# Performance work log

Measured on AMD Instinct MI355X. Metric: run time of the kernel, lower is better.

The kernel has to match this reference:

```python
import jax, jax.numpy as jnp
import numpy as np

N_NODES = 100000
N_EDGES = 1600000
IN_FEATS = 128
HID = 32
N_REL = 5
N_BASES = 2
N_PAIRS = 4096


def setup_inputs() -> dict:
    key = jax.random.key(0)
    ks = jax.random.split(key, 24)
    d = {}
    d['x'] = jax.random.normal(ks[0], (N_NODES, IN_FEATS), dtype=jnp.float32)
    d['edge_mask'] = jnp.ones((N_EDGES,), dtype=jnp.float32)
    d['etype'] = jax.random.randint(ks[1], (N_EDGES,), 0, N_REL, dtype=jnp.int32)
    d['src'] = jax.random.randint(ks[2], (N_EDGES,), 0, N_NODES, dtype=jnp.int32)
    d['dst'] = jax.random.randint(ks[3], (N_EDGES,), 0, N_NODES, dtype=jnp.int32)
    d['users_idx'] = jax.random.randint(ks[4], (N_PAIRS,), 0, N_NODES, dtype=jnp.int32)
    d['items_idx'] = jax.random.randint(ks[5], (N_PAIRS,), 0, N_NODES, dtype=jnp.int32)
    # RelGraphConv params (basis decomposition): layer1 in->32, layers 2,3 32->32
    def s(k, din):
        return 1.0 / np.sqrt(din)
    d['V1'] = jax.random.normal(ks[6], (N_BASES, IN_FEATS, HID), dtype=jnp.float32) * s(0, IN_FEATS)
    d['comp1'] = jax.random.normal(ks[7], (N_REL, N_BASES), dtype=jnp.float32)
    d['loop1'] = jax.random.normal(ks[8], (IN_FEATS, HID), dtype=jnp.float32) * s(0, IN_FEATS)
    d['b1'] = jnp.zeros((HID,), dtype=jnp.float32)
    d['V2'] = jax.random.normal(ks[9], (N_BASES, HID, HID), dtype=jnp.float32) * s(0, HID)
    d['comp2'] = jax.random.normal(ks[10], (N_REL, N_BASES), dtype=jnp.float32)
    d['loop2'] = jax.random.normal(ks[11], (HID, HID), dtype=jnp.float32) * s(0, HID)
    d['b2'] = jnp.zeros((HID,), dtype=jnp.float32)
    d['V3'] = jax.random.normal(ks[12], (N_BASES, HID, HID), dtype=jnp.float32) * s(0, HID)
    d['comp3'] = jax.random.normal(ks[13], (N_REL, N_BASES), dtype=jnp.float32)
    d['loop3'] = jax.random.normal(ks[14], (HID, HID), dtype=jnp.float32) * s(0, HID)
    d['b3'] = jnp.zeros((HID,), dtype=jnp.float32)
    # MLP head: lin1 (2*sum(latent_dim[1:]) = 192 -> 128), lin2 (128 -> 1)
    d['w1'] = jax.random.normal(ks[15], (2 * 3 * HID, 128), dtype=jnp.float32) * (1.0 / np.sqrt(2 * 3 * HID))
    d['bw1'] = jnp.zeros((128,), dtype=jnp.float32)
    d['w2'] = jax.random.normal(ks[16], (128, 1), dtype=jnp.float32) * (1.0 / np.sqrt(128))
    d['bw2'] = jnp.zeros((1,), dtype=jnp.float32)
    return d


def _rgcn_layer(x, V, comp, loopw, bias, etype, src, dst, norm):
    # basis-decomposed relational conv: W_r = sum_b comp[r,b] * V[b]
    xb = jnp.einsum('nd,bdo->nbo', x, V)                       # [N,B,O]
    msg = jnp.einsum('eb,ebo->eo', comp[etype], xb[src])       # [E,O]
    msg = msg * norm[:, None]                                  # edge_mask norm
    agg = jax.ops.segment_sum(msg, dst, num_segments=x.shape[0])
    return jnp.tanh(agg + x @ loopw + bias)


def reference(x, edge_mask, etype, src, dst, users_idx, items_idx,
              V1, comp1, loop1, b1, V2, comp2, loop2, b2, V3, comp3, loop3, b3,
              w1, bw1, w2, bw2):
    h1 = _rgcn_layer(x, V1, comp1, loop1, b1, etype, src, dst, edge_mask)
    h2 = _rgcn_layer(h1, V2, comp2, loop2, b2, etype, src, dst, edge_mask)
    h3 = _rgcn_layer(h2, V3, comp3, loop3, b3, etype, src, dst, edge_mask)
    concat_states = jnp.concatenate([h1, h2, h3], axis=1)      # [N, 96]
    feats = jnp.concatenate([concat_states[users_idx], concat_states[items_idx]], axis=1)  # [P,192]
    hidden = jax.nn.relu(feats @ w1 + bw1)
    out = hidden @ w2 + bw2
    return out[:, 0]  # multiply_by = 1
```

## Files before the change

### kernel.cpp

```cpp
#include <hip/hip_runtime.h>
#include <stdint.h>

#define N_NODES  100000
#define N_EDGES  1600000
#define IN_FEATS 128
#define HID      32
#define N_REL    5
#define N_BASES  2
#define N_PAIRS  4096

#define NB        196
#define BCAP      16384
#define EPB       2048
#define SC_BLOCKS 782
#define WP_BLOCKS 137
#define NBSORT    392
#define TD_BLOCKS 625

typedef __attribute__((ext_vector_type(8))) short short8;
typedef __attribute__((ext_vector_type(4))) float f32x4;

__device__ inline unsigned int pack_bf16(float a, float b) {
    unsigned int ua = __float_as_uint(a), ub = __float_as_uint(b);
    ua = (ua + 0x7fffu + ((ua >> 16) & 1u)) >> 16;
    ub = (ub + 0x7fffu + ((ub >> 16) & 1u)) >> 16;
    return ua | (ub << 16);
}

__device__ inline unsigned short bf16_1(float a) {
    unsigned int u = __float_as_uint(a);
    u = (u + 0x7fffu + ((u >> 16) & 1u)) >> 16;
    return (unsigned short)u;
}

__device__ inline void split_bf16_2(float a, float b, unsigned int& hi, unsigned int& lo) {
    unsigned int ha = bf16_1(a), hb = bf16_1(b);
    hi = ha | (hb << 16);
    float fa = __uint_as_float(ha << 16), fb = __uint_as_float(hb << 16);
    lo = pack_bf16(a - fa, b - fb);
}


#define SMEM_BYTES 23856

__global__ __launch_bounds__(256) void k_scatter_wprep(
    const int* __restrict__ src, const int* __restrict__ dst,
    const int* __restrict__ etype, const float* __restrict__ mask,
    int* __restrict__ gcur, int2* __restrict__ ebuf,
    const float* __restrict__ V1, const float* __restrict__ comp1, const float* __restrict__ loop1,
    const float* __restrict__ V2, const float* __restrict__ loop2,
    const float* __restrict__ V3, const float* __restrict__ loop3,
    unsigned short* __restrict__ Wbf1, unsigned short* __restrict__ Wcat2,
    unsigned short* __restrict__ Wcat3,
    const int* __restrict__ uidx, const int* __restrict__ iidx,
    unsigned char* __restrict__ flags) {
    __shared__ __attribute__((aligned(16))) char smem[SMEM_BYTES];
    int b = blockIdx.x;
    int t = threadIdx.x;
    if (b < SC_BLOCKS) {
        int2*  srec    = (int2*)smem;
        short* sb      = (short*)(smem + 16384);
        int*   lh      = (int*)(smem + 20480);
        int*   lex     = (int*)(smem + 21264);
        int*   gbase   = (int*)(smem + 22048);
        int*   scanbuf = (int*)(smem + 22832);
        int e0 = b * EPB;
        if (t < NB) lh[t] = 0;
        __syncthreads();
        int2 rec[8];
        int  bk[8];
#pragma unroll
        for (int i = 0; i < 8; i++) {
            int e = e0 + t + i * 256;
            if (e < N_EDGES) {
                int d = dst[e];
                bk[i] = d >> 9;
                rec[i].x = ((d & 511) << 23) | (src[e] << 4) | etype[e];
                rec[i].y = __float_as_int(mask[e]);
                atomicAdd(&lh[bk[i]], 1);
            } else bk[i] = -1;
        }
        __syncthreads();
        int cnt = (t < NB) ? lh[t] : 0;
        scanbuf[t] = cnt;
        __syncthreads();
        for (int off = 1; off < 256; off <<= 1) {
            int v = (t >= off) ? scanbuf[t - off] : 0;
            __syncthreads();
            scanbuf[t] += v;
            __syncthreads();
        }
        if (t < NB) {
            lex[t] = scanbuf[t] - cnt;
            gbase[t] = t * BCAP + (cnt ? atomicAdd(&gcur[t], cnt) : 0);
            lh[t] = 0;
        }
        __syncthreads();
#pragma unroll
        for (int i = 0; i < 8; i++) {
            if (bk[i] >= 0) {
                int p = lex[bk[i]] + atomicAdd(&lh[bk[i]], 1);
                srec[p] = rec[i];
                sb[p] = (short)bk[i];
            }
        }
        __syncthreads();
        int total = scanbuf[NB - 1];
        for (int idx = t; idx < total; idx += 256) {
            int bb = sb[idx];
            ebuf[gbase[bb] + (idx - lex[bb])] = srec[idx];
        }
        return;
    }
    int wb = b - SC_BLOCKS;
    if (wb == 136) {
        unsigned int* f4 = (unsigned int*)flags;
        for (int i = t; i < 25000; i += 256) f4[i] = 0u;
        __syncthreads();
        for (int i = t; i < N_PAIRS; i += 256) {
            flags[uidx[i]] = 1;
            flags[iidx[i]] = 1;
        }
        return;
    }
    if (wb < 96) {
        int idx = wb * 256 + t;
        if (idx >= 192 * IN_FEATS) return;
        int j = idx / IN_FEATS, k = idx % IN_FEATS;
        float v;
        if (j < 160) {
            int r = j >> 5, o = j & 31;
            v = comp1[r * 2 + 0] * V1[(size_t)(0 * IN_FEATS + k) * 32 + o]
              + comp1[r * 2 + 1] * V1[(size_t)(1 * IN_FEATS + k) * 32 + o];
        } else {
            v = loop1[k * 32 + (j - 160)];
        }
        Wbf1[idx] = bf16_1(v);
        return;
    }
    const float *V, *loopw;
    unsigned short* Wc;
    int idx;
    if (wb < 116) { V = V2; loopw = loop2; Wc = Wcat2; idx = (wb - 96) * 256 + t; }
    else          { V = V3; loopw = loop3; Wc = Wcat3; idx = (wb - 116) * 256 + t; }
    if (idx >= 32 * 160) return;
    int col = idx / 160, k = idx % 160;
    int seg = k >> 5, inner = k & 31;
    float v;
    if (seg < 2)      v = V[inner * 32 + col];
    else if (seg < 4) v = V[(32 + inner) * 32 + col];
    else              v = loopw[inner * 32 + col];
    Wc[idx] = bf16_1(v);
}


#define SMEM2_BYTES 19456

__global__ __launch_bounds__(512) void k_bsort_tl1(
    const int* __restrict__ gcur, const int2* __restrict__ ebuf,
    int2* __restrict__ esort, int* __restrict__ offsets,
    const float* __restrict__ xin,
    const unsigned short* __restrict__ Wbf, const float* __restrict__ bias,
    unsigned short* __restrict__ xs16, float* __restrict__ aggout) {
    __shared__ __attribute__((aligned(16))) char smem2[SMEM2_BYTES];
    int b = blockIdx.x;
    int t = threadIdx.x;
    if (b < NBSORT) {
        int* hist = (int*)smem2;
        int* incl = (int*)(smem2 + 2048);
        int* cur  = (int*)(smem2 + 4096);
        int* bs   = (int*)(smem2 + 6144);
        int* sBC  = (int*)(smem2 + 7168);
        int bb = b >> 1, h = b & 1;
        if (t < 256) bs[t] = (t < NB) ? gcur[t] : 0;
        __syncthreads();
        for (int off = 1; off < 256; off <<= 1) {
            int v = 0;
            if (t < 256 && t >= off) v = bs[t - off];
            __syncthreads();
            if (t < 256) bs[t] += v;
            __syncthreads();
        }
        if (t == 0) { sBC[1] = gcur[bb]; sBC[0] = bs[bb] - gcur[bb]; }
        hist[t] = 0;
        __syncthreads();
        int cnt = sBC[1], gbase = sBC[0];
        const int2* slab = ebuf + (size_t)bb * BCAP;
        for (int e = t; e < cnt; e += 512) {
            int dl = ((unsigned)slab[e].x) >> 23;
            atomicAdd(&hist[dl], 1);
        }
        __syncthreads();
        incl[t] = hist[t];
        __syncthreads();
        for (int off = 1; off < 512; off <<= 1) {
            int v = 0;
            if (t >= off) v = incl[t - off];
            __syncthreads();
            incl[t] += v;
            __syncthreads();
        }
        int ex = incl[t] - hist[t];
        cur[t] = ex;
        if ((t >> 8) == h) {
            int n = (bb << 9) + t;
            if (n <= N_NODES) offsets[n] = gbase + ex;
        }
        if (bb == NB - 1 && h == 1 && t == 0) offsets[N_NODES] = N_EDGES;
        __syncthreads();
        for (int e = t; e < cnt; e += 512) {
            int2 pk = slab[e];
            int dl = ((unsigned)pk.x) >> 23;
            if ((dl >> 8) == h) {
                int pos = gbase + atomicAdd(&cur[dl], 1);
                int2 rec;
                rec.x = pk.x & 0x7fffff;
                rec.y = pk.y;
                esort[pos] = rec;
            }
        }
        return;
    }
    int half = t >> 8;
    int tl   = t & 255;
    char* basep = smem2 + half * 9728;
    unsigned short* As = (unsigned short*)basep;
    unsigned short* tb = (unsigned short*)(basep + 4352);
    int bb = (b - NBSORT) * 2 + half;
    int wv = tl >> 6, lane = tl & 63;
    int q = lane >> 4, n16 = lane & 15;
    short8 bfr[3][4];
#pragma unroll
    for (int i = 0; i < 3; i++) {
        int tt = wv * 3 + i;
#pragma unroll
        for (int ks = 0; ks < 4; ks++)
            bfr[i][ks] = *(const short8*)(Wbf + (tt * 16 + n16) * 128 + ks * 32 + q * 8);
    }
    float bv0 = bias[n16], bv1 = bias[16 + n16];
    int node_l = tl >> 4;
    int seg    = tl & 15;
    int g0 = bb * 5;
    float4 p0, p1;
    {
        const float* xr = xin + ((size_t)(g0 * 16 + node_l)) * 128 + seg * 8;
        p0 = *(const float4*)xr;
        p1 = *(const float4*)(xr + 4);
    }
    for (int gi = 0; gi < 5; gi++) {
        int g = g0 + gi;
        int n0 = g * 16;
        __syncthreads();
        {
            uint4 v;
            v.x = pack_bf16(p0.x, p0.y);
            v.y = pack_bf16(p0.z, p0.w);
            v.z = pack_bf16(p1.x, p1.y);
            v.w = pack_bf16(p1.z, p1.w);
            *(uint4*)(As + node_l * 136 + seg * 8) = v;
        }
        __syncthreads();
        if (gi + 1 < 5) {
            const float* xr = xin + ((size_t)((g + 1) * 16 + node_l)) * 128 + seg * 8;
            p0 = *(const float4*)xr;
            p1 = *(const float4*)(xr + 4);
        }
        short8 afr[4];
#pragma unroll
        for (int ks = 0; ks < 4; ks++)
            afr[ks] = *(const short8*)(As + n16 * 136 + ks * 32 + q * 8);
        f32x4 d[3];
        f32x4 z = {0.f, 0.f, 0.f, 0.f};
#pragma unroll
        for (int i = 0; i < 3; i++) d[i] = z;
#pragma unroll
        for (int i = 0; i < 3; i++)
#pragma unroll
            for (int ks = 0; ks < 4; ks++)
                d[i] = __builtin_amdgcn_mfma_f32_16x16x32_bf16(afr[ks], bfr[i][ks], d[i], 0, 0, 0);
#pragma unroll
        for (int i = 0; i < 3; i++) {
            int tt = wv * 3 + i;
            if (tt < 10) {
#pragma unroll
                for (int r = 0; r < 4; r++)
                    tb[(q * 4 + r) * 168 + tt * 16 + n16] = bf16_1(d[i][r]);
            } else {
                float bv = (tt == 10) ? bv0 : bv1;
                int o = (tt - 10) * 16 + n16;
#pragma unroll
                for (int r = 0; r < 4; r++) {
                    int node = n0 + q * 4 + r;
                    aggout[(size_t)node * 32 + o] = d[i][r] + bv;
                }
            }
        }
        __syncthreads();
        for (int c = tl; c < 320; c += 256) {
            int node_i = c / 20, part = c % 20;
            short8 vv = *(const short8*)(tb + node_i * 168 + part * 8);
            *(short8*)(xs16 + (size_t)(n0 + node_i) * 160 + part * 8) = vv;
        }
    }
}


__global__ __launch_bounds__(256) void k_agg1(
    const int* __restrict__ offsets, const int2* __restrict__ esort,
    const unsigned int* __restrict__ xrel16, const float* __restrict__ agg,
    float* __restrict__ concat, unsigned int* __restrict__ hrel_out,
    const unsigned char* __restrict__ flags) {
    int v = blockIdx.x * 32 + (threadIdx.x >> 3);
    int o = threadIdx.x & 7;
    int s0 = offsets[v], s1 = offsets[v + 1];
    float4 a0 = *(const float4*)(agg + (size_t)v * 32 + o * 4);
    float acc0 = a0.x, acc1 = a0.y, acc2 = a0.z, acc3 = a0.w;
    int last = s1 - 1;
    for (int e = s0; e < s1; e += 16) {
        int addr[16];
        float m[16];
#pragma unroll
        for (int i = 0; i < 16; i++) {
            int ei = e + i;
            int ec = (ei <= last) ? ei : last;
            int2 pk = esort[ec];
            int low = pk.x;
            addr[i] = (low >> 4) * 80 + (low & 15) * 16;
            m[i] = (ei <= last) ? __int_as_float(pk.y) : 0.f;
        }
        uint2 xw[16];
#pragma unroll
        for (int i = 0; i < 16; i++)
            xw[i] = *(const uint2*)(xrel16 + (unsigned)addr[i] + o * 2);
#pragma unroll
        for (int i = 0; i < 16; i++) {
            float f0 = __uint_as_float(xw[i].x << 16);
            float f1 = __uint_as_float(xw[i].x & 0xffff0000u);
            float f2 = __uint_as_float(xw[i].y << 16);
            float f3 = __uint_as_float(xw[i].y & 0xffff0000u);
            acc0 = fmaf(m[i], f0, acc0);
            acc1 = fmaf(m[i], f1, acc1);
            acc2 = fmaf(m[i], f2, acc2);
            acc3 = fmaf(m[i], f3, acc3);
        }
    }
    float4 r;
    r.x = tanhf(acc0); r.y = tanhf(acc1); r.z = tanhf(acc2); r.w = tanhf(acc3);
    if (flags[v])
        *(float4*)(concat + (size_t)v * 96 + o * 4) = r;
    hrel_out[v * 16 + o * 2]     = pack_bf16(r.x, r.y);
    hrel_out[v * 16 + o * 2 + 1] = pack_bf16(r.z, r.w);
}


__global__ __launch_bounds__(256) void k_agg23(
    const int* __restrict__ offsets, const int2* __restrict__ esort,
    const unsigned int* __restrict__ hrel_in, const float* __restrict__ comp,
    const unsigned short* __restrict__ Wcat, const float* __restrict__ bias,
    float* __restrict__ concat, int hoff, unsigned int* __restrict__ hrel_out,
    const unsigned char* __restrict__ flags) {
    __shared__ unsigned int hbf[32][84];
    __shared__ float2 cLds[5];
    int t = threadIdx.x;
    if (t < 5) cLds[t] = ((const float2*)comp)[t];
    int nl = t >> 3;
    int v = blockIdx.x * 32 + nl;
    int o = t & 7;
    int s0 = offsets[v], s1 = offsets[v + 1];
    __syncthreads();
    float y00 = 0.f, y01 = 0.f, y02 = 0.f, y03 = 0.f;
    float y10 = 0.f, y11 = 0.f, y12 = 0.f, y13 = 0.f;
    int last = s1 - 1;
    for (int e = s0; e < s1; e += 16) {
        int addr[16];
        float c0[16], c1[16];
#pragma unroll
        for (int i = 0; i < 16; i++) {
            int ei = e + i;
            int ec = (ei <= last) ? ei : last;
            int2 pk = esort[ec];
            int low = pk.x;
            addr[i] = low & 0x7ffff0;
            float2 cc = cLds[low & 15];
            float m = (ei <= last) ? __int_as_float(pk.y) : 0.f;
            c0[i] = m * cc.x;
            c1[i] = m * cc.y;
        }
        uint2 xw[16];
#pragma unroll
        for (int i = 0; i < 16; i++)
            xw[i] = *(const uint2*)(hrel_in + (unsigned)addr[i] + o * 2);
#pragma unroll
        for (int i = 0; i < 16; i++) {
            float f0 = __uint_as_float(xw[i].x << 16);
            float f1 = __uint_as_float(xw[i].x & 0xffff0000u);
            float f2 = __uint_as_float(xw[i].y << 16);
            float f3 = __uint_as_float(xw[i].y & 0xffff0000u);
            y00 = fmaf(c0[i], f0, y00); y10 = fmaf(c1[i], f0, y10);
            y01 = fmaf(c0[i], f1, y01); y11 = fmaf(c1[i], f1, y11);
            y02 = fmaf(c0[i], f2, y02); y12 = fmaf(c1[i], f2, y12);
            y03 = fmaf(c0[i], f3, y03); y13 = fmaf(c1[i], f3, y13);
        }
    }
    unsigned int hi, lo;
    split_bf16_2(y00, y01, hi, lo);
    hbf[nl][o * 2]          = hi;  hbf[nl][16 + o * 2]     = lo;
    split_bf16_2(y02, y03, hi, lo);
    hbf[nl][o * 2 + 1]      = hi;  hbf[nl][16 + o * 2 + 1] = lo;
    split_bf16_2(y10, y11, hi, lo);
    hbf[nl][32 + o * 2]     = hi;  hbf[nl][48 + o * 2]     = lo;
    split_bf16_2(y12, y13, hi, lo);
    hbf[nl][32 + o * 2 + 1] = hi;  hbf[nl][48 + o * 2 + 1] = lo;
    *(uint2*)&hbf[nl][64 + o * 2] = *(const uint2*)(hrel_in + v * 16 + o * 2);
    __syncthreads();
    int wv = t >> 6, lane = t & 63;
    int q = lane >> 4, n16 = lane & 15;
    int gg = wv & 1;
    int tt = wv >> 1;
    f32x4 d = {0.f, 0.f, 0.f, 0.f};
#pragma unroll
    for (int ks = 0; ks < 5; ks++) {
        short8 afr = *(const short8*)&hbf[gg * 16 + n16][ks * 16 + q * 4];
        short8 bfr = *(const short8*)(Wcat + (tt * 16 + n16) * 160 + ks * 32 + q * 8);
        d = __builtin_amdgcn_mfma_f32_16x16x32_bf16(afr, bfr, d, 0, 0, 0);
    }
    float bv = bias[tt * 16 + n16];
    int n0 = blockIdx.x * 32 + gg * 16;
#pragma unroll
    for (int r = 0; r < 4; r++) {
        int node = n0 + q * 4 + r;
        float h = tanhf(d[r] + bv);
        if (flags[node])
            concat[(size_t)node * 96 + hoff + tt * 16 + n16] = h;
        if (hrel_out)
            ((unsigned short*)hrel_out)[node * 32 + tt * 16 + n16] = bf16_1(h);
    }
}


__global__ __launch_bounds__(256) void k_agg3s(
    const int* __restrict__ offsets, const int2* __restrict__ esort,
    const unsigned int* __restrict__ hrel_in, const float* __restrict__ comp,
    const unsigned short* __restrict__ Wcat, const float* __restrict__ bias,
    const int* __restrict__ uidx, const int* __restrict__ iidx,
    float* __restrict__ concat) {
    __shared__ unsigned int hbf[32][84];
    __shared__ float2 cLds[5];
    __shared__ int nlist[32];
    int t = threadIdx.x;
    if (t < 5) cLds[t] = ((const float2*)comp)[t];
    if (t < 32) {
        int slot = blockIdx.x * 32 + t;
        nlist[t] = (slot < N_PAIRS) ? uidx[slot] : iidx[slot - N_PAIRS];
    }
    __syncthreads();
    int nl = t >> 3;
    int v = nlist[nl];
    int o = t & 7;
    int s0 = offsets[v], s1 = offsets[v + 1];
    float y00 = 0.f, y01 = 0.f, y02 = 0.f, y03 = 0.f;
    float y10 = 0.f, y11 = 0.f, y12 = 0.f, y13 = 0.f;
    int last = s1 - 1;
    for (int e = s0; e < s1; e += 16) {
        int addr[16];
        float c0[16], c1[16];
#pragma unroll
        for (int i = 0; i < 16; i++) {
            int ei = e + i;
            int ec = (ei <= last) ? ei : last;
            int2 pk = esort[ec];
            int low = pk.x;
            addr[i] = low & 0x7ffff0;
            float2 cc = cLds[low & 15];
            float m = (ei <= last) ? __int_as_float(pk.y) : 0.f;
            c0[i] = m * cc.x;
            c1[i] = m * cc.y;
        }
        uint2 xw[16];
#pragma unroll
        for (int i = 0; i < 16; i++)
            xw[i] = *(const uint2*)(hrel_in + (unsigned)addr[i] + o * 2);
#pragma unroll
        for (int i = 0; i < 16; i++) {
            float f0 = __uint_as_float(xw[i].x << 16);
            float f1 = __uint_as_float(xw[i].x & 0xffff0000u);
            float f2 = __uint_as_float(xw[i].y << 16);
            float f3 = __uint_as_float(xw[i].y & 0xffff0000u);
            y00 = fmaf(c0[i], f0, y00); y10 = fmaf(c1[i], f0, y10);
            y01 = fmaf(c0[i], f1, y01); y11 = fmaf(c1[i], f1, y11);
            y02 = fmaf(c0[i], f2, y02); y12 = fmaf(c1[i], f2, y12);
            y03 = fmaf(c0[i], f3, y03); y13 = fmaf(c1[i], f3, y13);
        }
    }
    unsigned int hi, lo;
    split_bf16_2(y00, y01, hi, lo);
    hbf[nl][o * 2]          = hi;  hbf[nl][16 + o * 2]     = lo;
    split_bf16_2(y02, y03, hi, lo);
    hbf[nl][o * 2 + 1]      = hi;  hbf[nl][16 + o * 2 + 1] = lo;
    split_bf16_2(y10, y11, hi, lo);
    hbf[nl][32 + o * 2]     = hi;  hbf[nl][48 + o * 2]     = lo;
    split_bf16_2(y12, y13, hi, lo);
    hbf[nl][32 + o * 2 + 1] = hi;  hbf[nl][48 + o * 2 + 1] = lo;
    *(uint2*)&hbf[nl][64 + o * 2] = *(const uint2*)(hrel_in + v * 16 + o * 2);
    __syncthreads();
    int wv = t >> 6, lane = t & 63;
    int q = lane >> 4, n16 = lane & 15;
    int gg = wv & 1;
    int tt = wv >> 1;
    f32x4 d = {0.f, 0.f, 0.f, 0.f};
#pragma unroll
    for (int ks = 0; ks < 5; ks++) {
        short8 afr = *(const short8*)&hbf[gg * 16 + n16][ks * 16 + q * 4];
        short8 bfr = *(const short8*)(Wcat + (tt * 16 + n16) * 160 + ks * 32 + q * 8);
        d = __builtin_amdgcn_mfma_f32_16x16x32_bf16(afr, bfr, d, 0, 0, 0);
    }
    float bv = bias[tt * 16 + n16];
    int base = gg * 16 + q * 4;
#pragma unroll
    for (int r = 0; r < 4; r++) {
        int node = nlist[base + r];
        float h = tanhf(d[r] + bv);
        concat[(size_t)node * 96 + 64 + tt * 16 + n16] = h;
    }
}


__global__ void k_mlp(const float* __restrict__ concat, const int* __restrict__ uidx,
                      const int* __restrict__ iidx,
                      const float* __restrict__ w1, const float* __restrict__ bw1,
                      const float* __restrict__ w2, const float* __restrict__ bw2,
                      float* __restrict__ out) {
    __shared__ float feats[192];
    __shared__ float red[2];
    int p = blockIdx.x;
    int t = threadIdx.x;
    int u = uidx[p], it = iidx[p];
    for (int k = t; k < 192; k += 128)
        feats[k] = (k < 96) ? concat[(size_t)u * 96 + k] : concat[(size_t)it * 96 + (k - 96)];
    __syncthreads();
    float acc = bw1[t];
    for (int k = 0; k < 192; k++) acc += feats[k] * w1[k * 128 + t];
    float h = fmaxf(acc, 0.f);
    float part = h * w2[t];
    for (int off = 32; off > 0; off >>= 1) part += __shfl_down(part, off, 64);
    if ((t & 63) == 0) red[t >> 6] = part;
    __syncthreads();
    if (t == 0) out[p] = red[0] + red[1] + bw2[0];
}


extern "C" void kernel_launch(void* const* d_in, const int* in_sizes, int n_in,
                              void* d_out, int out_size, void* d_ws, size_t ws_size,
                              hipStream_t stream) {
    const float* x         = (const float*)d_in[0];
    const float* edge_mask = (const float*)d_in[1];
    const int*   etype     = (const int*)d_in[2];
    const int*   src       = (const int*)d_in[3];
    const int*   dst       = (const int*)d_in[4];
    const int*   users_idx = (const int*)d_in[5];
    const int*   items_idx = (const int*)d_in[6];
    const float* V1        = (const float*)d_in[7];
    const float* comp1     = (const float*)d_in[8];
    const float* loop1     = (const float*)d_in[9];
    const float* b1        = (const float*)d_in[10];
    const float* V2        = (const float*)d_in[11];
    const float* comp2     = (const float*)d_in[12];
    const float* loop2     = (const float*)d_in[13];
    const float* b2        = (const float*)d_in[14];
    const float* V3        = (const float*)d_in[15];
    const float* comp3     = (const float*)d_in[16];
    const float* loop3     = (const float*)d_in[17];
    const float* b3        = (const float*)d_in[18];
    const float* w1        = (const float*)d_in[19];
    const float* bw1       = (const float*)d_in[20];
    const float* w2        = (const float*)d_in[21];
    const float* bw2       = (const float*)d_in[22];
    float* out = (float*)d_out;

    uintptr_t w = (uintptr_t)d_ws;
    auto al = [&](size_t bytes) { uintptr_t p = (w + 255) & ~(uintptr_t)255; w = p + bytes; return p; };
    int*   gcur    = (int*)al(sizeof(int) * NB);
    unsigned char* flags = (unsigned char*)al(100000);
    int*   offsets = (int*)al(sizeof(int) * (N_NODES + 1));
    int2*  ebuf    = (int2*)al(sizeof(int2) * (size_t)NB * BCAP);
    unsigned int* xs16  = (unsigned int*)al(sizeof(unsigned int) * (size_t)N_NODES * 80);
    unsigned int* hrel1 = (unsigned int*)al(sizeof(unsigned int) * (size_t)N_NODES * 16);
    unsigned int* hrel2 = (unsigned int*)al(sizeof(unsigned int) * (size_t)N_NODES * 16);
    int2*  esort   = (int2*)al(sizeof(int2) * N_EDGES);
    unsigned short* Wbf1  = (unsigned short*)al(sizeof(unsigned short) * 192 * IN_FEATS);
    unsigned short* Wcat2 = (unsigned short*)al(sizeof(unsigned short) * 32 * 160);
    unsigned short* Wcat3 = (unsigned short*)al(sizeof(unsigned short) * 32 * 160);
    float* aggA    = (float*)al(sizeof(float) * (size_t)N_NODES * 32);
    float* concat  = (float*)al(sizeof(float) * (size_t)N_NODES * 96);

    hipMemsetAsync(gcur, 0, sizeof(int) * NB, stream);

    k_scatter_wprep<<<SC_BLOCKS + WP_BLOCKS, 256, 0, stream>>>(
        src, dst, etype, edge_mask, gcur, ebuf,
        V1, comp1, loop1, V2, loop2, V3, loop3, Wbf1, Wcat2, Wcat3,
        users_idx, items_idx, flags);
    k_bsort_tl1<<<NBSORT + TD_BLOCKS, 512, 0, stream>>>(
        gcur, ebuf, esort, offsets,
        x, Wbf1, b1, (unsigned short*)xs16, aggA);

    const int agrid = N_NODES / 32;

    k_agg1<<<agrid, 256, 0, stream>>>(offsets, esort, xs16, aggA, concat, hrel1, flags);
    k_agg23<<<agrid, 256, 0, stream>>>(offsets, esort, hrel1, comp2, Wcat2, b2,
                                       concat, 32, hrel2, flags);
    k_agg3s<<<256, 256, 0, stream>>>(offsets, esort, hrel2, comp3, Wcat3, b3,
                                     users_idx, items_idx, concat);

    k_mlp<<<N_PAIRS, 128, 0, stream>>>(concat, users_idx, items_idx, w1, bw1, w2, bw2, out);
}
```

Measured before the change: 300.2 us.

## Restrict layer-2 aggregation to neighbours of query pair nodes

While aggregating layer 1, pair nodes mark their source neighbours in a second flag array. A compaction kernel builds a node list from it, and the layer-2 kernel processes only those nodes. This avoids layer-2 work for nodes whose outputs layer 3 never reads. The cost is an extra launch, atomic compaction with unordered node lists that can reduce locality, and scattered byte stores during layer 1.

```diff
diff --git a/kernel.cpp b/kernel.cpp
--- a/kernel.cpp
+++ b/kernel.cpp
@@ -53,7 +53,8 @@
     unsigned short* __restrict__ Wbf1, unsigned short* __restrict__ Wcat2,
     unsigned short* __restrict__ Wcat3,
     const int* __restrict__ uidx, const int* __restrict__ iidx,
-    unsigned char* __restrict__ flags) {
+    unsigned char* __restrict__ flags, unsigned char* __restrict__ flag2,
+    int* __restrict__ cnt2) {
     __shared__ __attribute__((aligned(16))) char smem[SMEM_BYTES];
     int b = blockIdx.x;
     int t = threadIdx.x;
@@ -115,11 +116,14 @@
     int wb = b - SC_BLOCKS;
     if (wb == 136) {
         unsigned int* f4 = (unsigned int*)flags;
-        for (int i = t; i < 25000; i += 256) f4[i] = 0u;
+        unsigned int* g4 = (unsigned int*)flag2;
+        for (int i = t; i < 25000; i += 256) { f4[i] = 0u; g4[i] = 0u; }
+        if (t == 0) *cnt2 = 0;
         __syncthreads();
         for (int i = t; i < N_PAIRS; i += 256) {
-            flags[uidx[i]] = 1;
-            flags[iidx[i]] = 1;
+            int u = uidx[i], it = iidx[i];
+            flags[u] = 1; flags[it] = 1;
+            flag2[u] = 1; flag2[it] = 1;
         }
         return;
     }
@@ -309,10 +313,11 @@
     const int* __restrict__ offsets, const int2* __restrict__ esort,
     const unsigned int* __restrict__ xrel16, const float* __restrict__ agg,
     float* __restrict__ concat, unsigned int* __restrict__ hrel_out,
-    const unsigned char* __restrict__ flags) {
+    const unsigned char* __restrict__ flags, unsigned char* __restrict__ flag2) {
     int v = blockIdx.x * 32 + (threadIdx.x >> 3);
     int o = threadIdx.x & 7;
     int s0 = offsets[v], s1 = offsets[v + 1];
+    bool fmark = flags[v] && (o == 0);
     float4 a0 = *(const float4*)(agg + (size_t)v * 32 + o * 4);
     float acc0 = a0.x, acc1 = a0.y, acc2 = a0.z, acc3 = a0.w;
     int last = s1 - 1;
@@ -327,6 +332,7 @@
             int low = pk.x;
             addr[i] = (low >> 4) * 80 + (low & 15) * 16;
             m[i] = (ei <= last) ? __int_as_float(pk.y) : 0.f;
+            if (fmark && ei <= last) flag2[(unsigned)low >> 4] = 1;
         }
         uint2 xw[16];
 #pragma unroll
@@ -353,21 +359,40 @@
 }
 
 
-__global__ __launch_bounds__(256) void k_agg23(
+__global__ __launch_bounds__(256) void k_compact(
+    const unsigned char* __restrict__ flag2, int* __restrict__ nlist2,
+    int* __restrict__ cnt2) {
+    int i = blockIdx.x * 256 + threadIdx.x;
+    if (i < N_NODES && flag2[i]) {
+        int pos = atomicAdd(cnt2, 1);
+        nlist2[pos] = i;
+    }
+}
+
+
+__global__ __launch_bounds__(256) void k_agg2c(
     const int* __restrict__ offsets, const int2* __restrict__ esort,
     const unsigned int* __restrict__ hrel_in, const float* __restrict__ comp,
     const unsigned short* __restrict__ Wcat, const float* __restrict__ bias,
-    float* __restrict__ concat, int hoff, unsigned int* __restrict__ hrel_out,
-    const unsigned char* __restrict__ flags) {
+    float* __restrict__ concat, unsigned int* __restrict__ hrel_out,
+    const unsigned char* __restrict__ flags,
+    const int* __restrict__ nlist2, const int* __restrict__ cnt2) {
+    int cnt = *cnt2;
+    if (blockIdx.x * 32 >= cnt) return;
     __shared__ unsigned int hbf[32][84];
     __shared__ float2 cLds[5];
+    __shared__ int nlist[32];
     int t = threadIdx.x;
     if (t < 5) cLds[t] = ((const float2*)comp)[t];
+    if (t < 32) {
+        int slot = blockIdx.x * 32 + t;
+        nlist[t] = nlist2[(slot < cnt) ? slot : 0];
+    }
+    __syncthreads();
     int nl = t >> 3;
-    int v = blockIdx.x * 32 + nl;
+    int v = nlist[nl];
     int o = t & 7;
     int s0 = offsets[v], s1 = offsets[v + 1];
-    __syncthreads();
     float y00 = 0.f, y01 = 0.f, y02 = 0.f, y03 = 0.f;
     float y10 = 0.f, y11 = 0.f, y12 = 0.f, y13 = 0.f;
     int last = s1 - 1;
@@ -425,15 +450,14 @@
         d = __builtin_amdgcn_mfma_f32_16x16x32_bf16(afr, bfr, d, 0, 0, 0);
     }
     float bv = bias[tt * 16 + n16];
-    int n0 = blockIdx.x * 32 + gg * 16;
+    int base = gg * 16 + q * 4;
 #pragma unroll
     for (int r = 0; r < 4; r++) {
-        int node = n0 + q * 4 + r;
+        int node = nlist[base + r];
         float h = tanhf(d[r] + bv);
         if (flags[node])
-            concat[(size_t)node * 96 + hoff + tt * 16 + n16] = h;
-        if (hrel_out)
-            ((unsigned short*)hrel_out)[node * 32 + tt * 16 + n16] = bf16_1(h);
+            concat[(size_t)node * 96 + 32 + tt * 16 + n16] = h;
+        ((unsigned short*)hrel_out)[node * 32 + tt * 16 + n16] = bf16_1(h);
     }
 }
 
@@ -581,6 +605,9 @@
     auto al = [&](size_t bytes) { uintptr_t p = (w + 255) & ~(uintptr_t)255; w = p + bytes; return p; };
     int*   gcur    = (int*)al(sizeof(int) * NB);
     unsigned char* flags = (unsigned char*)al(100000);
+    unsigned char* flag2 = (unsigned char*)al(100000);
+    int*   cnt2    = (int*)al(sizeof(int));
+    int*   nlist2  = (int*)al(sizeof(int) * N_NODES);
     int*   offsets = (int*)al(sizeof(int) * (N_NODES + 1));
     int2*  ebuf    = (int2*)al(sizeof(int2) * (size_t)NB * BCAP);
     unsigned int* xs16  = (unsigned int*)al(sizeof(unsigned int) * (size_t)N_NODES * 80);
@@ -598,16 +625,18 @@
     k_scatter_wprep<<<SC_BLOCKS + WP_BLOCKS, 256, 0, stream>>>(
         src, dst, etype, edge_mask, gcur, ebuf,
         V1, comp1, loop1, V2, loop2, V3, loop3, Wbf1, Wcat2, Wcat3,
-        users_idx, items_idx, flags);
+        users_idx, items_idx, flags, flag2, cnt2);
     k_bsort_tl1<<<NBSORT + TD_BLOCKS, 512, 0, stream>>>(
         gcur, ebuf, esort, offsets,
         x, Wbf1, b1, (unsigned short*)xs16, aggA);
 
     const int agrid = N_NODES / 32;
 
-    k_agg1<<<agrid, 256, 0, stream>>>(offsets, esort, xs16, aggA, concat, hrel1, flags);
-    k_agg23<<<agrid, 256, 0, stream>>>(offsets, esort, hrel1, comp2, Wcat2, b2,
-                                       concat, 32, hrel2, flags);
+    k_agg1<<<agrid, 256, 0, stream>>>(offsets, esort, xs16, aggA, concat, hrel1,
+                                      flags, flag2);
+    k_compact<<<(N_NODES + 255) / 256, 256, 0, stream>>>(flag2, nlist2, cnt2);
+    k_agg2c<<<agrid, 256, 0, stream>>>(offsets, esort, hrel1, comp2, Wcat2, b2,
+                                       concat, hrel2, flags, nlist2, cnt2);
     k_agg3s<<<256, 256, 0, stream>>>(offsets, esort, hrel2, comp3, Wcat3, b3,
                                      users_idx, items_idx, concat);
 
```

Result: slower. 342.1 us (+14.0%).
